# Performance work log

Measured on AMD Instinct MI355X. Metric: run time of the kernel, lower is better.

The kernel has to match this reference:

```python
import jax, jax.numpy as jnp
from jax import lax
import numpy as np

EPS = 1e-5


def ref_points(Hk, Wk):
    # torch linspace(0.5, Hk-0.5, Hk)/Hk * 2 - 1, stacked (y, x)
    ys = (jnp.linspace(0.5, Hk - 0.5, Hk) / Hk) * 2.0 - 1.0
    xs = (jnp.linspace(0.5, Wk - 0.5, Wk) / Wk) * 2.0 - 1.0
    yy, xx = jnp.meshgrid(ys, xs, indexing='ij')
    return jnp.stack([yy, xx], axis=-1)  # (Hk, Wk, 2) in (y, x) order


def grid_sample(img, grid):
    # Bilinear, align_corners=True, zeros padding (torch F.grid_sample defaults).
    # img: (N, C, Hi, Wi); grid: (N, Hg, Wg, 2) with (x, y) in [-1, 1].
    N, C, Hi, Wi = img.shape
    Hg, Wg = grid.shape[1], grid.shape[2]
    gx = (grid[..., 0] + 1.0) * 0.5 * (Wi - 1)
    gy = (grid[..., 1] + 1.0) * 0.5 * (Hi - 1)
    x0 = jnp.floor(gx)
    y0 = jnp.floor(gy)
    wx1 = gx - x0
    wy1 = gy - y0
    imgf = img.reshape(N, C, Hi * Wi)

    def corner(ix, iy, w):
        valid = (ix >= 0) & (ix < Wi) & (iy >= 0) & (iy < Hi)
        idx = (jnp.clip(iy, 0, Hi - 1).astype(jnp.int32) * Wi
               + jnp.clip(ix, 0, Wi - 1).astype(jnp.int32)).reshape(N, -1)
        vals = jax.vmap(lambda im, f: im[:, f])(imgf, idx)  # (N, C, Hg*Wg)
        return vals * (w * valid).reshape(N, 1, -1)

    out = (corner(x0, y0, (1 - wx1) * (1 - wy1))
           + corner(x0 + 1, y0, wx1 * (1 - wy1))
           + corner(x0, y0 + 1, (1 - wx1) * wy1)
           + corner(x0 + 1, y0 + 1, wx1 * wy1))
    return out.reshape(N, C, Hg, Wg)


def setup_inputs() -> dict:
    key = jax.random.key(0)
    ks = jax.random.split(key, 8)
    B, C, H, W = 8, 128, 64, 64
    gc, nH = 64, 4
    return {
        'x': jax.random.normal(ks[0], (B, C, H, W), jnp.float32),
        'w_dw': jax.random.normal(ks[1], (gc, 1, 5, 5), jnp.float32) * 0.1,
        'ln_w': jnp.ones((gc,), jnp.float32),
        'w_off': jax.random.normal(ks[2], (3, gc), jnp.float32) * 0.1,
        'wq': jax.random.normal(ks[3], (C, C), jnp.float32) * 0.05,
        'wk': jax.random.normal(ks[4], (C, C), jnp.float32) * 0.05,
        'wv': jax.random.normal(ks[5], (C, C), jnp.float32) * 0.05,
        'wo': jax.random.normal(ks[6], (C, C), jnp.float32) * 0.05,
        'rpe': jax.random.normal(ks[7], (nH, 2 * H - 1, 2 * W - 1), jnp.float32) * 0.01,
    }


def reference(x, w_dw, ln_w, w_off, wq, wk, wv, wo, rpe):
    B, C, H, W = x.shape
    G, nH = 2, 4
    gc = C // G           # group channels
    dh = C // nH          # head channels
    gh = nH // G          # heads per group
    scale = dh ** -0.5
    orf = 1.0             # offset_range_factor

    conv1x1 = lambda t, w: jnp.einsum('oi,bihw->bohw', w, t)

    q = conv1x1(x, wq)                                    # (B, C, H, W)
    q_off = q.reshape(B * G, gc, H, W)

    # conv_offset: depthwise 5x5 stride 4 pad 2 -> BiasFree LN (over C) -> GELU -> 1x1 to 3
    off = lax.conv_general_dilated(q_off, w_dw, (4, 4), ((2, 2), (2, 2)),
                                   dimension_numbers=('NCHW', 'OIHW', 'NCHW'),
                                   feature_group_count=gc)  # (B*G, gc, Hk, Wk)
    var = jnp.var(off, axis=1, keepdims=True)
    off = off / jnp.sqrt(var + EPS) * ln_w.reshape(1, -1, 1, 1)
    off = jax.nn.gelu(off, approximate=False)
    off = jnp.einsum('oi,bihw->bohw', w_off, off)          # (B*G, 3, Hk, Wk)

    Hk, Wk = off.shape[2], off.shape[3]
    n = Hk * Wk

    # channel 0 = y offset, channel 1 = x offset, channel 2 = modulation
    offset = jnp.stack([jnp.tanh(off[:, 0]) * (orf / Hk),
                        jnp.tanh(off[:, 1]) * (orf / Wk)], axis=-1)  # (B*G, Hk, Wk, 2) (y,x)
    dm = jax.nn.sigmoid(off[:, 2])[:, None]                # (B*G, 1, Hk, Wk)

    pos = offset + ref_points(Hk, Wk)[None]                # (B*G, Hk, Wk, 2) (y,x)

    xs = grid_sample(x.reshape(B * G, gc, H, W), pos[..., ::-1])  # grid in (x,y)
    xs = (xs * dm).reshape(B, C, 1, n)

    k = conv1x1(xs, wk).reshape(B * nH, dh, n)
    v = conv1x1(xs, wv).reshape(B * nH, dh, n)
    qf = q.reshape(B * nH, dh, H * W)

    attn = jnp.einsum('bcm,bcn->bmn', qf, k) * scale       # (B*nH, H*W, n)

    # relative-position bias sampled at continuous displacements
    rpe_b = jnp.broadcast_to(rpe[None], (B, nH, 2 * H - 1, 2 * W - 1)
                             ).reshape(B * G, gh, 2 * H - 1, 2 * W - 1)
    qg = ref_points(H, W).reshape(H * W, 2)                # (H*W, 2)
    disp = (qg[None, :, None, :] - pos.reshape(B * G, 1, n, 2)) * 0.5  # (B*G, H*W, n, 2)
    bias = grid_sample(rpe_b, disp[..., ::-1]).reshape(B * nH, H * W, n)

    attn = jax.nn.softmax(attn + bias, axis=2)
    out = jnp.einsum('bmn,bcn->bcm', attn, v).reshape(B, C, H, W)
    return conv1x1(out, wo)
```

## Files before the change

kernel.cpp:

```cpp
#include <hip/hip_runtime.h>
#include <hip/hip_bf16.h>
#include <math.h>

#define HW 4096
#define NCH 128

typedef __attribute__((ext_vector_type(8))) short short8;
typedef __attribute__((ext_vector_type(4))) float f32x4;

__device__ __forceinline__ short f2bf(float f) {
  union { __hip_bfloat16 h; short s; } u;
  u.h = __float2bfloat16(f);
  return u.s;
}
__device__ __forceinline__ float bf2f(short s) {
  union { unsigned u; float f; } u;
  u.u = ((unsigned)(unsigned short)s) << 16;
  return u.f;
}

__global__ __launch_bounds__(256) void wcvt_kernel(
    const float* __restrict__ wq, const float* __restrict__ wk,
    const float* __restrict__ wv, const float* __restrict__ wo,
    short* __restrict__ wq_hi, short* __restrict__ wq_lo,
    short* __restrict__ wk_bf, short* __restrict__ wv_bf,
    short* __restrict__ wo_bf) {
  int i = blockIdx.x * 256 + threadIdx.x;
  float q = wq[i];
  short h = f2bf(q);
  wq_hi[i] = h;
  wq_lo[i] = f2bf(q - bf2f(h));
  wk_bf[i] = f2bf(wk[i]);
  wv_bf[i] = f2bf(wv[i]);
  wo_bf[i] = f2bf(wo[i]);
}

__global__ __launch_bounds__(256) void rpe_pad_kernel(
    const float* __restrict__ rpe, _Float16* __restrict__ rpe16) {
  int i = blockIdx.x * 256 + threadIdx.x;
  if (i >= 4 * 16800) return;
  int h = i / 16800, r = i % 16800;
  int y = r / 130, x = r % 130;
  float v = 0.f;
  if (y >= 1 && y <= 127 && x >= 1 && x <= 127)
    v = rpe[(size_t)h * (127 * 127) + (y - 1) * 127 + (x - 1)];
  rpe16[i] = (_Float16)v;
}

__global__ __launch_bounds__(256) void xcvt_kernel(const float* __restrict__ x,
                                                   short* __restrict__ xhi,
                                                   short* __restrict__ xlo) {
  __shared__ float s[64][65];
  int b = blockIdx.z;
  int c0 = blockIdx.y * 64;
  int m0 = blockIdx.x * 64;
  int tid = threadIdx.x;
  {
    int ml = tid & 63, ch = tid >> 6;
#pragma unroll
    for (int i = 0; i < 16; ++i) {
      int cl = i * 4 + ch;
      s[cl][ml] = x[((size_t)(b * NCH + c0 + cl)) * HW + m0 + ml];
    }
  }
  __syncthreads();
  {
    int cl = tid & 63, mh = tid >> 6;
#pragma unroll
    for (int i = 0; i < 16; ++i) {
      int ml = i * 4 + mh;
      float v = s[cl][ml];
      short hi = f2bf(v);
      short lo = f2bf(v - bf2f(hi));
      size_t idx = ((size_t)(b * HW + m0 + ml)) * NCH + c0 + cl;
      xhi[idx] = hi;
      xlo[idx] = lo;
    }
  }
}

__global__ __launch_bounds__(256) void qmfma_kernel(
    const short* __restrict__ xhi, const short* __restrict__ xlo,
    const short* __restrict__ whi, const short* __restrict__ wlo,
    float* __restrict__ qT) {
  int tid = threadIdx.x;
  int w = tid >> 6, lane = tid & 63, l15 = lane & 15, qd = lane >> 4;
  int b = blockIdx.y;
  int m0 = blockIdx.x * 64 + w * 16;

  f32x4 acc[8];
#pragma unroll
  for (int ot = 0; ot < 8; ++ot) acc[ot] = (f32x4){0.f, 0.f, 0.f, 0.f};

  size_t arow = ((size_t)(b * HW + m0 + l15)) * NCH + qd * 8;
#pragma unroll
  for (int kc = 0; kc < 4; ++kc) {
    short8 ah = *(const short8*)&xhi[arow + kc * 32];
    short8 al = *(const short8*)&xlo[arow + kc * 32];
#pragma unroll
    for (int ot = 0; ot < 8; ++ot) {
      size_t wrow = (size_t)(ot * 16 + l15) * NCH + kc * 32 + qd * 8;
      short8 bh = *(const short8*)&whi[wrow];
      short8 bl = *(const short8*)&wlo[wrow];
      acc[ot] = __builtin_amdgcn_mfma_f32_16x16x32_bf16(ah, bh, acc[ot], 0, 0, 0);
      acc[ot] = __builtin_amdgcn_mfma_f32_16x16x32_bf16(al, bh, acc[ot], 0, 0, 0);
      acc[ot] = __builtin_amdgcn_mfma_f32_16x16x32_bf16(ah, bl, acc[ot], 0, 0, 0);
    }
  }
#pragma unroll
  for (int ot = 0; ot < 8; ++ot)
#pragma unroll
    for (int r = 0; r < 4; ++r)
      qT[((size_t)(b * HW + m0 + qd * 4 + r)) * NCH + ot * 16 + l15] = acc[ot][r];
}

__device__ __forceinline__ float wsum64(float v) {
#pragma unroll
  for (int o = 32; o > 0; o >>= 1) v += __shfl_xor(v, o);
  return v;
}

__global__ __launch_bounds__(64) void conv_offset_kernel(
    const float* __restrict__ qT, const float* __restrict__ w_dw,
    const float* __restrict__ ln_w, const float* __restrict__ w_off,
    float* __restrict__ pos, float* __restrict__ dm) {
  int c = threadIdx.x;
  int p = blockIdx.x;
  int bg = blockIdx.y;
  int py = p >> 4, px = p & 15;
  const float* qp = qT + (size_t)(bg >> 1) * HW * NCH + (bg & 1) * 64 + c;
  const float* wd = w_dw + c * 25;
  float acc = 0.f;
#pragma unroll
  for (int ky = 0; ky < 5; ++ky) {
    int iy = 4 * py + ky - 2;
    if (iy < 0 || iy >= 64) continue;
#pragma unroll
    for (int kx = 0; kx < 5; ++kx) {
      int ix = 4 * px + kx - 2;
      if (ix < 0 || ix >= 64) continue;
      acc += wd[ky * 5 + kx] * qp[(size_t)(iy * 64 + ix) * NCH];
    }
  }
  float mean = wsum64(acc) * (1.f / 64.f);
  float msq = wsum64(acc * acc) * (1.f / 64.f);
  float var = msq - mean * mean;
  float g = acc * rsqrtf(var + 1e-5f) * ln_w[c];
  g = 0.5f * g * (1.f + erff(g * 0.70710678118654752f));
  float o0 = wsum64(w_off[c] * g);
  float o1 = wsum64(w_off[64 + c] * g);
  float o2 = wsum64(w_off[128 + c] * g);
  if (c == 0) {
    int idx = bg * 256 + p;
    pos[idx * 2] = tanhf(o0) * (1.f / 16.f) + ((py + 0.5f) * (1.f / 8.f) - 1.f);
    pos[idx * 2 + 1] = tanhf(o1) * (1.f / 16.f) + ((px + 0.5f) * (1.f / 8.f) - 1.f);
    dm[idx] = 1.f / (1.f + expf(-o2));
  }
}

__global__ __launch_bounds__(256) void sample_xs_kernel(
    const short* __restrict__ xhi, const short* __restrict__ xlo,
    const float* __restrict__ pos, const float* __restrict__ dm,
    short* __restrict__ xsT) {
  int tid = threadIdx.x;
  int c = tid & 63, w = tid >> 6;
  int bg = blockIdx.x;
  int p0 = blockIdx.y * 16 + w * 4;
  int b = bg >> 1, ch0 = (bg & 1) * 64;
  size_t rb = (size_t)b * HW * NCH + ch0 + c;
#pragma unroll
  for (int i = 0; i < 4; ++i) {
    int p = p0 + i;
    int idx = bg * 256 + p;
    float posy = pos[idx * 2], posx = pos[idx * 2 + 1];
    float dmv = dm[idx];
    float gx = (posx + 1.f) * 31.5f;
    float gy = (posy + 1.f) * 31.5f;
    float x0f = floorf(gx), y0f = floorf(gy);
    int ix = (int)x0f, iy = (int)y0f;
    float fx = gx - x0f, fy = gy - y0f;
    float w00 = (1.f - fx) * (1.f - fy), w10 = fx * (1.f - fy);
    float w01 = (1.f - fx) * fy, w11 = fx * fy;
    bool vx0 = (ix >= 0 && ix < 64), vx1 = (ix + 1 >= 0 && ix + 1 < 64);
    bool vy0 = (iy >= 0 && iy < 64), vy1 = (iy + 1 >= 0 && iy + 1 < 64);
    if (!(vx0 && vy0)) w00 = 0.f;
    if (!(vx1 && vy0)) w10 = 0.f;
    if (!(vx0 && vy1)) w01 = 0.f;
    if (!(vx1 && vy1)) w11 = 0.f;
    int x0c = min(max(ix, 0), 63), x1c = min(max(ix + 1, 0), 63);
    int y0c = min(max(iy, 0), 63), y1c = min(max(iy + 1, 0), 63);
    size_t i00 = rb + (size_t)(y0c * 64 + x0c) * NCH;
    size_t i10 = rb + (size_t)(y0c * 64 + x1c) * NCH;
    size_t i01 = rb + (size_t)(y1c * 64 + x0c) * NCH;
    size_t i11 = rb + (size_t)(y1c * 64 + x1c) * NCH;
    float v = w00 * (bf2f(xhi[i00]) + bf2f(xlo[i00])) +
              w10 * (bf2f(xhi[i10]) + bf2f(xlo[i10])) +
              w01 * (bf2f(xhi[i01]) + bf2f(xlo[i01])) +
              w11 * (bf2f(xhi[i11]) + bf2f(xlo[i11]));
    xsT[((size_t)(b * 256 + p)) * NCH + ch0 + c] = f2bf(v * dmv);
  }
}

__global__ __launch_bounds__(256) void kv_mfma_kernel(
    const short* __restrict__ xsT, const short* __restrict__ wk_bf,
    const short* __restrict__ wv_bf, short* __restrict__ kbf,
    short* __restrict__ vbf) {
  int tid = threadIdx.x;
  int w = tid >> 6, lane = tid & 63, l15 = lane & 15, qd = lane >> 4;
  int bh = blockIdx.x, b = bh >> 2;
  int n0 = blockIdx.y * 128;
  f32x4 acc[2][2];
#pragma unroll
  for (int t = 0; t < 2; ++t)
#pragma unroll
    for (int ot = 0; ot < 2; ++ot) acc[t][ot] = (f32x4){0.f, 0.f, 0.f, 0.f};

  if (blockIdx.z == 0) {
#pragma unroll
    for (int t = 0; t < 2; ++t) {
      int nt = w * 2 + t;
      size_t arow = ((size_t)(b * 256 + n0 + nt * 16 + l15)) * NCH + qd * 8;
#pragma unroll
      for (int kc = 0; kc < 4; ++kc) {
        short8 a = *(const short8*)&xsT[arow + kc * 32];
#pragma unroll
        for (int ot = 0; ot < 2; ++ot) {
          short8 bb = *(const short8*)&wk_bf[(size_t)(bh % 4 * 32 + ot * 16 + l15) * NCH + kc * 32 + qd * 8];
          acc[t][ot] = __builtin_amdgcn_mfma_f32_16x16x32_bf16(a, bb, acc[t][ot], 0, 0, 0);
        }
      }
    }
#pragma unroll
    for (int t = 0; t < 2; ++t)
#pragma unroll
      for (int ot = 0; ot < 2; ++ot)
#pragma unroll
        for (int r = 0; r < 4; ++r)
          kbf[((size_t)(bh * 256 + n0 + (w * 2 + t) * 16 + qd * 4 + r)) * 32 +
              ot * 16 + l15] = f2bf(acc[t][ot][r]);
  } else {
#pragma unroll
    for (int t = 0; t < 2; ++t) {
      int nt = w * 2 + t;
      size_t brow = ((size_t)(b * 256 + n0 + nt * 16 + l15)) * NCH + qd * 8;
#pragma unroll
      for (int kc = 0; kc < 4; ++kc) {
        short8 bb = *(const short8*)&xsT[brow + kc * 32];
#pragma unroll
        for (int ot = 0; ot < 2; ++ot) {
          short8 a = *(const short8*)&wv_bf[(size_t)(bh % 4 * 32 + ot * 16 + l15) * NCH + kc * 32 + qd * 8];
          acc[t][ot] = __builtin_amdgcn_mfma_f32_16x16x32_bf16(a, bb, acc[t][ot], 0, 0, 0);
        }
      }
    }
#pragma unroll
    for (int t = 0; t < 2; ++t)
#pragma unroll
      for (int ot = 0; ot < 2; ++ot)
#pragma unroll
        for (int r = 0; r < 4; ++r)
          vbf[((size_t)(bh * 32 + ot * 16 + qd * 4 + r)) * 256 + n0 +
              (w * 2 + t) * 16 + l15] = f2bf(acc[t][ot][r]);
  }
}

#define PROW 264
#define POS_OFF 33552
#define LDS_BYTES 35600

__global__ __launch_bounds__(256) void attn_kernel(
    const float* __restrict__ qT, const short* __restrict__ kbf,
    const short* __restrict__ vbf, const float* __restrict__ pos,
    const _Float16* __restrict__ rpe16, short* __restrict__ outT) {
  __shared__ __align__(16) unsigned char s_raw[LDS_BYTES];
  _Float16* tab = (_Float16*)s_raw;
  float* s_pos = (float*)(s_raw + POS_OFF);
  short* s_p = (short*)s_raw;

  int tid = threadIdx.x;
  int wv = tid >> 6;
  int lane = tid & 63;
  int l15 = lane & 15;
  int qd = lane >> 4;
  int bh = blockIdx.y;
  int b = bh >> 2, h = bh & 3;
  int bg = b * 2 + (h >> 1);
  int m0 = blockIdx.x * 64 + wv * 16;

  {
    const uint4* src = (const uint4*)(rpe16 + (size_t)h * 16800);
    uint4* dst = (uint4*)s_raw;
    for (int i = tid; i < 2097; i += 256) dst[i] = src[i];
    const float* posg = pos + (size_t)bg * 512;
    s_pos[tid] = posg[tid];
    s_pos[256 + tid] = posg[256 + tid];
  }

  short8 qfrag;
  {
    const float* qg = qT + ((size_t)(b * HW + m0 + l15)) * NCH + h * 32 + qd * 8;
    f32x4 a0 = *(const f32x4*)qg;
    f32x4 a1 = *(const f32x4*)(qg + 4);
#pragma unroll
    for (int j = 0; j < 4; ++j) {
      qfrag[j] = f2bf(a0[j]);
      qfrag[4 + j] = f2bf(a1[j]);
    }
  }

  f32x4 acc[16];
  {
    const short* kb = kbf + ((size_t)bh * 256 + l15) * 32 + qd * 8;
#pragma unroll
    for (int t = 0; t < 16; ++t) {
      short8 kf = *(const short8*)(kb + t * 16 * 32);
      acc[t] = __builtin_amdgcn_mfma_f32_16x16x32_bf16(
          kf, qfrag, (f32x4){0.f, 0.f, 0.f, 0.f}, 0, 0, 0);
    }
  }
  __syncthreads();

  int m = m0 + l15;
  float gy0 = ((((float)(m >> 6) + 0.5f) * (1.f / 32.f) - 1.f) * 0.5f + 1.f) * 63.f;
  float gx0 = ((((float)(m & 63) + 0.5f) * (1.f / 32.f) - 1.f) * 0.5f + 1.f) * 63.f;
  float mx = -1e30f;
#pragma unroll
  for (int t = 0; t < 16; ++t) {
#pragma unroll
    for (int r = 0; r < 4; ++r) {
      int n = t * 16 + qd * 4 + r;
      float2 pp = *(const float2*)&s_pos[n * 2];
      float gy = gy0 - pp.x * 31.5f;
      float gx = gx0 - pp.y * 31.5f;
      float y0f = floorf(gy), x0f = floorf(gx);
      float fy = gy - y0f, fx = gx - x0f;
      int base = (int)y0f * 130 + (int)x0f + 131;
      float t00 = (float)tab[base], t10 = (float)tab[base + 1];
      float t01 = (float)tab[base + 130], t11 = (float)tab[base + 131];
      float r0 = t00 + fx * (t10 - t00);
      float r1 = t01 + fx * (t11 - t01);
      float bias = r0 + fy * (r1 - r0);
      float s = acc[t][r] * 0.17677669529663688f + bias;
      acc[t][r] = s;
      mx = fmaxf(mx, s);
    }
  }
  mx = fmaxf(mx, __shfl_xor(mx, 16));
  float M = fmaxf(mx, __shfl_xor(mx, 32));

  float sm = 0.f;
#pragma unroll
  for (int t = 0; t < 16; ++t) {
#pragma unroll
    for (int r = 0; r < 4; ++r) {
      float e = __expf(acc[t][r] - M);
      acc[t][r] = e;
      sm += e;
    }
  }
  sm += __shfl_xor(sm, 16);
  sm += __shfl_xor(sm, 32);
  float inv = 1.f / sm;

  __syncthreads();

  {
    short* pw = s_p + wv * 16 * PROW + l15 * PROW;
#pragma unroll
    for (int t = 0; t < 16; ++t) {
      int n = t * 16 + qd * 4;
      short4 pk;
      pk.x = f2bf(acc[t][0] * inv);
      pk.y = f2bf(acc[t][1] * inv);
      pk.z = f2bf(acc[t][2] * inv);
      pk.w = f2bf(acc[t][3] * inv);
      *(short4*)(pw + n) = pk;
    }
  }

  f32x4 o0 = {0.f, 0.f, 0.f, 0.f}, o1 = {0.f, 0.f, 0.f, 0.f};
  {
    const short* vb = vbf + ((size_t)bh * 32 + l15) * 256 + qd * 8;
    const short* pr = s_p + wv * 16 * PROW + l15 * PROW + qd * 8;
#pragma unroll
    for (int ch = 0; ch < 8; ++ch) {
      short8 pf = *(const short8*)(pr + ch * 32);
      short8 v0 = *(const short8*)(vb + ch * 32);
      short8 v1 = *(const short8*)(vb + 16 * 256 + ch * 32);
      o0 = __builtin_amdgcn_mfma_f32_16x16x32_bf16(v0, pf, o0, 0, 0, 0);
      o1 = __builtin_amdgcn_mfma_f32_16x16x32_bf16(v1, pf, o1, 0, 0, 0);
    }
  }
  {
    size_t row = (size_t)(b * HW + m0 + l15) * NCH + h * 32 + qd * 4;
    short4 s0, s1;
    s0.x = f2bf(o0[0]); s0.y = f2bf(o0[1]); s0.z = f2bf(o0[2]); s0.w = f2bf(o0[3]);
    s1.x = f2bf(o1[0]); s1.y = f2bf(o1[1]); s1.z = f2bf(o1[2]); s1.w = f2bf(o1[3]);
    *(short4*)&outT[row] = s0;
    *(short4*)&outT[row + 16] = s1;
  }
}

__global__ __launch_bounds__(256) void wo_mfma_kernel(
    const short* __restrict__ attnT, const short* __restrict__ wo_bf,
    float* __restrict__ out) {
  int tid = threadIdx.x;
  int wv = tid >> 6;
  int lane = tid & 63;
  int l15 = lane & 15;
  int qd = lane >> 4;
  int b = blockIdx.x >> 6;
  int m0 = (blockIdx.x & 63) * 64 + wv * 16;

  f32x4 acc[8];
#pragma unroll
  for (int ot = 0; ot < 8; ++ot) acc[ot] = (f32x4){0.f, 0.f, 0.f, 0.f};

  const short* arow = attnT + (size_t)(b * HW + m0 + l15) * NCH + qd * 8;
  const short* wrow = wo_bf + (size_t)l15 * NCH + qd * 8;
#pragma unroll
  for (int kc = 0; kc < 4; ++kc) {
    short8 afrag = *(const short8*)(arow + kc * 32);
#pragma unroll
    for (int ot = 0; ot < 8; ++ot) {
      short8 bfrag = *(const short8*)(wrow + (size_t)ot * 16 * NCH + kc * 32);
      acc[ot] = __builtin_amdgcn_mfma_f32_16x16x32_bf16(afrag, bfrag, acc[ot],
                                                        0, 0, 0);
    }
  }
#pragma unroll
  for (int ot = 0; ot < 8; ++ot) {
    float* op = out + ((size_t)b * NCH + ot * 16 + l15) * HW + m0 + qd * 4;
    *(f32x4*)op = acc[ot];
  }
}

extern "C" void kernel_launch(void* const* d_in, const int* in_sizes, int n_in,
                              void* d_out, int out_size, void* d_ws,
                              size_t ws_size, hipStream_t stream) {
  const float* x = (const float*)d_in[0];
  const float* w_dw = (const float*)d_in[1];
  const float* ln_w = (const float*)d_in[2];
  const float* w_off = (const float*)d_in[3];
  const float* wq = (const float*)d_in[4];
  const float* wk = (const float*)d_in[5];
  const float* wv = (const float*)d_in[6];
  const float* wo = (const float*)d_in[7];
  const float* rpe = (const float*)d_in[8];
  float* out = (float*)d_out;

  float* qT = out;
  short* sb = (short*)d_ws;
  short* xhi = sb;
  short* outT = sb;
  short* xlo = sb + 4194304;
  short* xsT = sb + 8388608;
  short* kbf = sb + 8650752;
  short* vbf = sb + 8912896;
  short* wq_hi = sb + 9175040;
  short* wq_lo = sb + 9191424;
  short* wk_bf = sb + 9207808;
  short* wv_bf = sb + 9224192;
  short* wo_bf = sb + 9240576;
  _Float16* rpe16 = (_Float16*)(sb + 9256960);
  float* pos = (float*)(sb + 9324160);
  float* dm = pos + 8192;

  wcvt_kernel<<<64, 256, 0, stream>>>(wq, wk, wv, wo, wq_hi, wq_lo, wk_bf,
                                      wv_bf, wo_bf);
  rpe_pad_kernel<<<263, 256, 0, stream>>>(rpe, rpe16);
  xcvt_kernel<<<dim3(64, 2, 8), 256, 0, stream>>>(x, xhi, xlo);
  qmfma_kernel<<<dim3(64, 8), 256, 0, stream>>>(xhi, xlo, wq_hi, wq_lo, qT);
  conv_offset_kernel<<<dim3(256, 16), 64, 0, stream>>>(qT, w_dw, ln_w, w_off,
                                                       pos, dm);
  sample_xs_kernel<<<dim3(16, 16), 256, 0, stream>>>(xhi, xlo, pos, dm, xsT);
  kv_mfma_kernel<<<dim3(32, 2, 2), 256, 0, stream>>>(xsT, wk_bf, wv_bf, kbf,
                                                     vbf);
  attn_kernel<<<dim3(64, 32), 256, 0, stream>>>(qT, kbf, vbf, pos, rpe16,
                                                outT);
  wo_mfma_kernel<<<512, 256, 0, stream>>>(outT, wo_bf, out);
}
```

Measured before the change: 191.7 us.

## Fuse prep kernels and x-convert with Q projection, pack hi/lo bf16

Merges the weight-convert and rpe-pad kernels into one launch, and fuses the x transpose/convert with the Q projection MFMA so the A fragments are built from shared memory rather than re-read from global. x hi/lo bf16 halves are packed into one 32-bit word so bilinear sampling issues one load per corner instead of two. It also regroups conv_offset into 256-thread blocks and vectorises the position and rpe-table reads in the attention kernel. The cost is more shared memory per block in the fused Q kernel and unaligned 4-byte table loads.

```diff
diff --git a/kernel.cpp b/kernel.cpp
--- a/kernel.cpp
+++ b/kernel.cpp
@@ -18,85 +18,85 @@
   u.u = ((unsigned)(unsigned short)s) << 16;
   return u.f;
 }
-
-__global__ __launch_bounds__(256) void wcvt_kernel(
+__device__ __forceinline__ float upk(unsigned u) {
+  union { unsigned u; float f; } a, b;
+  a.u = u & 0xFFFF0000u;
+  b.u = u << 16;
+  return a.f + b.f;
+}
+
+__global__ __launch_bounds__(256) void prep_kernel(
     const float* __restrict__ wq, const float* __restrict__ wk,
     const float* __restrict__ wv, const float* __restrict__ wo,
-    short* __restrict__ wq_hi, short* __restrict__ wq_lo,
-    short* __restrict__ wk_bf, short* __restrict__ wv_bf,
-    short* __restrict__ wo_bf) {
-  int i = blockIdx.x * 256 + threadIdx.x;
-  float q = wq[i];
-  short h = f2bf(q);
-  wq_hi[i] = h;
-  wq_lo[i] = f2bf(q - bf2f(h));
-  wk_bf[i] = f2bf(wk[i]);
-  wv_bf[i] = f2bf(wv[i]);
-  wo_bf[i] = f2bf(wo[i]);
-}
-
-__global__ __launch_bounds__(256) void rpe_pad_kernel(
-    const float* __restrict__ rpe, _Float16* __restrict__ rpe16) {
-  int i = blockIdx.x * 256 + threadIdx.x;
-  if (i >= 4 * 16800) return;
-  int h = i / 16800, r = i % 16800;
-  int y = r / 130, x = r % 130;
-  float v = 0.f;
-  if (y >= 1 && y <= 127 && x >= 1 && x <= 127)
-    v = rpe[(size_t)h * (127 * 127) + (y - 1) * 127 + (x - 1)];
-  rpe16[i] = (_Float16)v;
-}
-
-__global__ __launch_bounds__(256) void xcvt_kernel(const float* __restrict__ x,
-                                                   short* __restrict__ xhi,
-                                                   short* __restrict__ xlo) {
-  __shared__ float s[64][65];
-  int b = blockIdx.z;
-  int c0 = blockIdx.y * 64;
+    const float* __restrict__ rpe, short* __restrict__ wq_hi,
+    short* __restrict__ wq_lo, short* __restrict__ wk_bf,
+    short* __restrict__ wv_bf, short* __restrict__ wo_bf,
+    _Float16* __restrict__ rpe16) {
+  if (blockIdx.x < 64) {
+    int i = blockIdx.x * 256 + threadIdx.x;
+    float q = wq[i];
+    short h = f2bf(q);
+    wq_hi[i] = h;
+    wq_lo[i] = f2bf(q - bf2f(h));
+    wk_bf[i] = f2bf(wk[i]);
+    wv_bf[i] = f2bf(wv[i]);
+    wo_bf[i] = f2bf(wo[i]);
+  } else {
+    int i = (blockIdx.x - 64) * 256 + threadIdx.x;
+    if (i >= 4 * 16800) return;
+    int h = i / 16800, r = i % 16800;
+    int y = r / 130, x = r % 130;
+    float v = 0.f;
+    if (y >= 1 && y <= 127 && x >= 1 && x <= 127)
+      v = rpe[(size_t)h * (127 * 127) + (y - 1) * 127 + (x - 1)];
+    rpe16[i] = (_Float16)v;
+  }
+}
+
+__global__ __launch_bounds__(256) void xq_kernel(
+    const float* __restrict__ x, const short* __restrict__ whi,
+    const short* __restrict__ wlo, unsigned* __restrict__ xpk,
+    float* __restrict__ qT) {
+  __shared__ float s[128][65];
+  int tid = threadIdx.x;
+  int b = blockIdx.y;
   int m0 = blockIdx.x * 64;
-  int tid = threadIdx.x;
   {
     int ml = tid & 63, ch = tid >> 6;
 #pragma unroll
-    for (int i = 0; i < 16; ++i) {
-      int cl = i * 4 + ch;
-      s[cl][ml] = x[((size_t)(b * NCH + c0 + cl)) * HW + m0 + ml];
+    for (int i = 0; i < 32; ++i) {
+      int c = i * 4 + ch;
+      s[c][ml] = x[((size_t)(b * NCH + c)) * HW + m0 + ml];
     }
   }
   __syncthreads();
   {
-    int cl = tid & 63, mh = tid >> 6;
-#pragma unroll
-    for (int i = 0; i < 16; ++i) {
-      int ml = i * 4 + mh;
-      float v = s[cl][ml];
+    int c = tid & 127, mh = tid >> 7;
+#pragma unroll
+    for (int i = 0; i < 32; ++i) {
+      int m = i * 2 + mh;
+      float v = s[c][m];
       short hi = f2bf(v);
-      short lo = f2bf(v - bf2f(hi));
-      size_t idx = ((size_t)(b * HW + m0 + ml)) * NCH + c0 + cl;
-      xhi[idx] = hi;
-      xlo[idx] = lo;
-    }
-  }
-}
-
-__global__ __launch_bounds__(256) void qmfma_kernel(
-    const short* __restrict__ xhi, const short* __restrict__ xlo,
-    const short* __restrict__ whi, const short* __restrict__ wlo,
-    float* __restrict__ qT) {
-  int tid = threadIdx.x;
+      unsigned lo = (unsigned short)f2bf(v - bf2f(hi));
+      xpk[((size_t)(b * HW + m0 + m)) * NCH + c] =
+          (((unsigned)(unsigned short)hi) << 16) | lo;
+    }
+  }
   int w = tid >> 6, lane = tid & 63, l15 = lane & 15, qd = lane >> 4;
-  int b = blockIdx.y;
-  int m0 = blockIdx.x * 64 + w * 16;
-
+  int mrow = w * 16 + l15;
   f32x4 acc[8];
 #pragma unroll
   for (int ot = 0; ot < 8; ++ot) acc[ot] = (f32x4){0.f, 0.f, 0.f, 0.f};
-
-  size_t arow = ((size_t)(b * HW + m0 + l15)) * NCH + qd * 8;
 #pragma unroll
   for (int kc = 0; kc < 4; ++kc) {
-    short8 ah = *(const short8*)&xhi[arow + kc * 32];
-    short8 al = *(const short8*)&xlo[arow + kc * 32];
+    short8 ah, al;
+#pragma unroll
+    for (int j = 0; j < 8; ++j) {
+      float v = s[kc * 32 + qd * 8 + j][mrow];
+      short hi = f2bf(v);
+      ah[j] = hi;
+      al[j] = f2bf(v - bf2f(hi));
+    }
 #pragma unroll
     for (int ot = 0; ot < 8; ++ot) {
       size_t wrow = (size_t)(ot * 16 + l15) * NCH + kc * 32 + qd * 8;
@@ -111,7 +111,8 @@
   for (int ot = 0; ot < 8; ++ot)
 #pragma unroll
     for (int r = 0; r < 4; ++r)
-      qT[((size_t)(b * HW + m0 + qd * 4 + r)) * NCH + ot * 16 + l15] = acc[ot][r];
+      qT[((size_t)(b * HW + m0 + w * 16 + qd * 4 + r)) * NCH + ot * 16 + l15] =
+          acc[ot][r];
 }
 
 __device__ __forceinline__ float wsum64(float v) {
@@ -120,12 +121,12 @@
   return v;
 }
 
-__global__ __launch_bounds__(64) void conv_offset_kernel(
+__global__ __launch_bounds__(256) void conv_offset_kernel(
     const float* __restrict__ qT, const float* __restrict__ w_dw,
     const float* __restrict__ ln_w, const float* __restrict__ w_off,
     float* __restrict__ pos, float* __restrict__ dm) {
-  int c = threadIdx.x;
-  int p = blockIdx.x;
+  int c = threadIdx.x & 63;
+  int p = blockIdx.x * 4 + (threadIdx.x >> 6);
   int bg = blockIdx.y;
   int py = p >> 4, px = p & 15;
   const float* qp = qT + (size_t)(bg >> 1) * HW * NCH + (bg & 1) * 64 + c;
@@ -159,9 +160,8 @@
 }
 
 __global__ __launch_bounds__(256) void sample_xs_kernel(
-    const short* __restrict__ xhi, const short* __restrict__ xlo,
-    const float* __restrict__ pos, const float* __restrict__ dm,
-    short* __restrict__ xsT) {
+    const unsigned* __restrict__ xpk, const float* __restrict__ pos,
+    const float* __restrict__ dm, short* __restrict__ xsT) {
   int tid = threadIdx.x;
   int c = tid & 63, w = tid >> 6;
   int bg = blockIdx.x;
@@ -189,14 +189,10 @@
     if (!(vx1 && vy1)) w11 = 0.f;
     int x0c = min(max(ix, 0), 63), x1c = min(max(ix + 1, 0), 63);
     int y0c = min(max(iy, 0), 63), y1c = min(max(iy + 1, 0), 63);
-    size_t i00 = rb + (size_t)(y0c * 64 + x0c) * NCH;
-    size_t i10 = rb + (size_t)(y0c * 64 + x1c) * NCH;
-    size_t i01 = rb + (size_t)(y1c * 64 + x0c) * NCH;
-    size_t i11 = rb + (size_t)(y1c * 64 + x1c) * NCH;
-    float v = w00 * (bf2f(xhi[i00]) + bf2f(xlo[i00])) +
-              w10 * (bf2f(xhi[i10]) + bf2f(xlo[i10])) +
-              w01 * (bf2f(xhi[i01]) + bf2f(xlo[i01])) +
-              w11 * (bf2f(xhi[i11]) + bf2f(xlo[i11]));
+    float v = w00 * upk(xpk[rb + (size_t)(y0c * 64 + x0c) * NCH]) +
+              w10 * upk(xpk[rb + (size_t)(y0c * 64 + x1c) * NCH]) +
+              w01 * upk(xpk[rb + (size_t)(y1c * 64 + x0c) * NCH]) +
+              w11 * upk(xpk[rb + (size_t)(y1c * 64 + x1c) * NCH]);
     xsT[((size_t)(b * 256 + p)) * NCH + ch0 + c] = f2bf(v * dmv);
   }
 }
@@ -218,14 +214,13 @@
   if (blockIdx.z == 0) {
 #pragma unroll
     for (int t = 0; t < 2; ++t) {
-      int nt = w * 2 + t;
-      size_t arow = ((size_t)(b * 256 + n0 + nt * 16 + l15)) * NCH + qd * 8;
+      size_t arow = ((size_t)(b * 256 + n0 + (w * 2 + t) * 16 + l15)) * NCH + qd * 8;
 #pragma unroll
       for (int kc = 0; kc < 4; ++kc) {
         short8 a = *(const short8*)&xsT[arow + kc * 32];
 #pragma unroll
         for (int ot = 0; ot < 2; ++ot) {
-          short8 bb = *(const short8*)&wk_bf[(size_t)(bh % 4 * 32 + ot * 16 + l15) * NCH + kc * 32 + qd * 8];
+          short8 bb = *(const short8*)&wk_bf[(size_t)((bh % 4) * 32 + ot * 16 + l15) * NCH + kc * 32 + qd * 8];
           acc[t][ot] = __builtin_amdgcn_mfma_f32_16x16x32_bf16(a, bb, acc[t][ot], 0, 0, 0);
         }
       }
@@ -241,14 +236,13 @@
   } else {
 #pragma unroll
     for (int t = 0; t < 2; ++t) {
-      int nt = w * 2 + t;
-      size_t brow = ((size_t)(b * 256 + n0 + nt * 16 + l15)) * NCH + qd * 8;
+      size_t brow = ((size_t)(b * 256 + n0 + (w * 2 + t) * 16 + l15)) * NCH + qd * 8;
 #pragma unroll
       for (int kc = 0; kc < 4; ++kc) {
         short8 bb = *(const short8*)&xsT[brow + kc * 32];
 #pragma unroll
         for (int ot = 0; ot < 2; ++ot) {
-          short8 a = *(const short8*)&wv_bf[(size_t)(bh % 4 * 32 + ot * 16 + l15) * NCH + kc * 32 + qd * 8];
+          short8 a = *(const short8*)&wv_bf[(size_t)((bh % 4) * 32 + ot * 16 + l15) * NCH + kc * 32 + qd * 8];
           acc[t][ot] = __builtin_amdgcn_mfma_f32_16x16x32_bf16(a, bb, acc[t][ot], 0, 0, 0);
         }
       }
@@ -326,21 +320,30 @@
   float mx = -1e30f;
 #pragma unroll
   for (int t = 0; t < 16; ++t) {
+    const f32x4* pp4 = (const f32x4*)&s_pos[(t * 16 + qd * 4) * 2];
+    f32x4 pA = pp4[0];
+    f32x4 pB = pp4[1];
+    float py[4] = {pA[0], pA[2], pB[0], pB[2]};
+    float px[4] = {pA[1], pA[3], pB[1], pB[3]};
 #pragma unroll
     for (int r = 0; r < 4; ++r) {
-      int n = t * 16 + qd * 4 + r;
-      float2 pp = *(const float2*)&s_pos[n * 2];
-      float gy = gy0 - pp.x * 31.5f;
-      float gx = gx0 - pp.y * 31.5f;
+      float gy = gy0 - py[r] * 31.5f;
+      float gx = gx0 - px[r] * 31.5f;
       float y0f = floorf(gy), x0f = floorf(gx);
       float fy = gy - y0f, fx = gx - x0f;
       int base = (int)y0f * 130 + (int)x0f + 131;
-      float t00 = (float)tab[base], t10 = (float)tab[base + 1];
-      float t01 = (float)tab[base + 130], t11 = (float)tab[base + 131];
+      unsigned u0, u1;
+      __builtin_memcpy(&u0, (const char*)tab + 2 * base, 4);
+      __builtin_memcpy(&u1, (const char*)tab + 2 * base + 260, 4);
+      union { unsigned u; _Float16 h[2]; } c0, c1;
+      c0.u = u0;
+      c1.u = u1;
+      float t00 = (float)c0.h[0], t10 = (float)c0.h[1];
+      float t01 = (float)c1.h[0], t11 = (float)c1.h[1];
       float r0 = t00 + fx * (t10 - t00);
       float r1 = t01 + fx * (t11 - t01);
       float bias = r0 + fy * (r1 - r0);
-      float s = acc[t][r] * 0.17677669529663688f + bias;
+      float s = fmaf(acc[t][r], 0.17677669529663688f, bias);
       acc[t][r] = s;
       mx = fmaxf(mx, s);
     }
@@ -451,9 +454,8 @@
 
   float* qT = out;
   short* sb = (short*)d_ws;
-  short* xhi = sb;
+  unsigned* xpk = (unsigned*)sb;
   short* outT = sb;
-  short* xlo = sb + 4194304;
   short* xsT = sb + 8388608;
   short* kbf = sb + 8650752;
   short* vbf = sb + 8912896;
@@ -466,14 +468,12 @@
   float* pos = (float*)(sb + 9324160);
   float* dm = pos + 8192;
 
-  wcvt_kernel<<<64, 256, 0, stream>>>(wq, wk, wv, wo, wq_hi, wq_lo, wk_bf,
-                                      wv_bf, wo_bf);
-  rpe_pad_kernel<<<263, 256, 0, stream>>>(rpe, rpe16);
-  xcvt_kernel<<<dim3(64, 2, 8), 256, 0, stream>>>(x, xhi, xlo);
-  qmfma_kernel<<<dim3(64, 8), 256, 0, stream>>>(xhi, xlo, wq_hi, wq_lo, qT);
-  conv_offset_kernel<<<dim3(256, 16), 64, 0, stream>>>(qT, w_dw, ln_w, w_off,
+  prep_kernel<<<327, 256, 0, stream>>>(wq, wk, wv, wo, rpe, wq_hi, wq_lo,
+                                       wk_bf, wv_bf, wo_bf, rpe16);
+  xq_kernel<<<dim3(64, 8), 256, 0, stream>>>(x, wq_hi, wq_lo, xpk, qT);
+  conv_offset_kernel<<<dim3(64, 16), 256, 0, stream>>>(qT, w_dw, ln_w, w_off,
                                                        pos, dm);
-  sample_xs_kernel<<<dim3(16, 16), 256, 0, stream>>>(xhi, xlo, pos, dm, xsT);
+  sample_xs_kernel<<<dim3(16, 16), 256, 0, stream>>>(xpk, pos, dm, xsT);
   kv_mfma_kernel<<<dim3(32, 2, 2), 256, 0, stream>>>(xsT, wk_bf, wv_bf, kbf,
                                                      vbf);
   attn_kernel<<<dim3(64, 32), 256, 0, stream>>>(qT, kbf, vbf, pos, rpe16,
```

Result: faster. 185.2 us (-3.4%).
